# Performance work log

Measured on AMD Instinct MI355X. Metric: run time of the kernel, lower is better.

The kernel has to match this reference:

```python
import jax, jax.numpy as jnp
import numpy as np

N = 100000      # nodes
E = 1600000     # edges (avg degree 16)
IN = 128        # in_channels
H = 128         # hidden_channels
OUT = 64        # out_channels
NHID = 3        # num_layers (hidden->hidden SAGE convs)


def _lin(k, fan_out, fan_in):
    s = 1.0 / np.sqrt(fan_in)
    return jax.random.uniform(k, (fan_out, fan_in), jnp.float32, -s, s)


def setup_inputs() -> dict:
    key = jax.random.key(0)
    ks = jax.random.split(key, 12)
    x = jax.random.normal(ks[0], (N, IN), dtype=jnp.float32)
    edge_index = jax.random.randint(ks[1], (2, E), 0, N, dtype=jnp.int32)
    # inProj Linear(IN -> H)
    Wp = _lin(ks[2], H, IN)
    bp = jnp.zeros((H,), jnp.float32)
    # 3 hidden SAGEConv(H -> H): lin_l (with bias) on aggregated neighbors, lin_r (no bias) on root
    Wl_h = jnp.stack([_lin(jax.random.fold_in(ks[3], i), H, H) for i in range(NHID)])
    bl_h = jnp.zeros((NHID, H), jnp.float32)
    Wr_h = jnp.stack([_lin(jax.random.fold_in(ks[4], i), H, H) for i in range(NHID)])
    # output SAGEConv(H -> OUT)
    Wl_o = _lin(ks[5], OUT, H)
    bl_o = jnp.zeros((OUT,), jnp.float32)
    Wr_o = _lin(ks[6], OUT, H)
    return {"x": x, "edge_index": edge_index, "Wp": Wp, "bp": bp,
            "Wl_h": Wl_h, "bl_h": bl_h, "Wr_h": Wr_h,
            "Wl_o": Wl_o, "bl_o": bl_o, "Wr_o": Wr_o}


def reference(x, edge_index, Wp, bp, Wl_h, bl_h, Wr_h, Wl_o, bl_o, Wr_o):
    src, dst = edge_index[0], edge_index[1]
    ones = jnp.ones((E,), x.dtype)
    deg = jax.ops.segment_sum(ones, dst, num_segments=N)           # [N]
    inv_deg = (1.0 / jnp.maximum(deg, 1.0))[:, None]               # [N,1]

    def sage(h, Wl, bl, Wr):
        # mean aggregation of source features onto destinations (irregular gather+scatter)
        s = jax.ops.segment_sum(h[src], dst, num_segments=N)       # [N,d]
        mean = s * inv_deg
        return mean @ Wl.T + bl + h @ Wr.T

    h = x @ Wp.T + bp
    inp = h
    h = jax.nn.relu(h)
    for i in range(NHID):
        h = sage(h, Wl_h[i], bl_h[i], Wr_h[i])
        h = jax.nn.relu(h)                                          # dropout is identity in eval
        h = h + 0.2 * inp
    h = sage(h, Wl_o, bl_o, Wr_o)
    return jax.nn.log_softmax(h, axis=-1)
```

## Files before the change

### kernel.cpp

```cpp
#include <hip/hip_runtime.h>
#include <math.h>

#define N_NODES 100000
#define N_EDGES 1600000
#define NBUK 391
#define PCHUNK 8192
#define NPBLK 196
#define GBLK32 3125

typedef unsigned short u16;
typedef unsigned char u8;
typedef __bf16 bf16x8 __attribute__((ext_vector_type(8)));
typedef float f32x4 __attribute__((ext_vector_type(4)));
typedef float f32x2 __attribute__((ext_vector_type(2)));

#define OFF_RP      0u
#define OFF_INVDEG  400016u
#define OFF_BHIST   800016u
#define OFF_BBASE   801600u
#define OFF_GCUR    803200u
#define OFF_PCTR    804800u
#define OFF_PAIRS   805056u
#define OFF_COL     13605056u
#define OFF_PACK    20005056u
#define OFF_INP     20267200u
#define OFF_H       45867200u
#define OFF_H8A     71467200u
#define OFF_H8B     84267200u
#define OFF_GL      97067200u
#define OFF_GR      109867200u
#define OFF_MEAN    122667200u
#define WS_NEEDED   148267200u

#define PK_WP   0
#define PK_WL   16384
#define PK_WR   65536
#define PK_WLO  114688
#define PK_WRO  122880

__device__ __forceinline__ float bfl(unsigned u) {
  union { unsigned i; float f; } v; v.i = u << 16; return v.f;
}
__device__ __forceinline__ float bfh(unsigned u) {
  union { unsigned i; float f; } v; v.i = u & 0xFFFF0000u; return v.f;
}
__device__ __forceinline__ u16 f2b(float f) {
  union { float f; unsigned i; } v; v.f = f;
  unsigned r = (v.i + 0x7FFFu + ((v.i >> 16) & 1u)) >> 16;
  return (u16)r;
}

__global__ __launch_bounds__(256) void pack_weights_k(
    const float* __restrict__ Wp, const float* __restrict__ Wl,
    const float* __restrict__ Wr, const float* __restrict__ Wlo,
    const float* __restrict__ Wro, u16* __restrict__ P) {
  int t = blockIdx.x * 256 + threadIdx.x;
  if (t >= 16384) return;
  const float* W; u16* dst; int j; int NT;
  if (t < 2048)        { W = Wp;                    dst = P + PK_WP;                j = t;                 NT = 8; }
  else if (t < 8192)   { int m = (t - 2048) >> 11;  j = (t - 2048) & 2047;
                         W = Wl + (m << 14);        dst = P + PK_WL + (m << 14);    NT = 8; }
  else if (t < 14336)  { int m = (t - 8192) >> 11;  j = (t - 8192) & 2047;
                         W = Wr + (m << 14);        dst = P + PK_WR + (m << 14);    NT = 8; }
  else if (t < 15360)  { j = t - 14336;             W = Wlo;  dst = P + PK_WLO;     NT = 4; }
  else                 { j = t - 15360;             W = Wro;  dst = P + PK_WRO;     NT = 4; }
  int lane = j & 63;
  int nt, kt;
  if (NT == 8) { nt = (j >> 6) & 7; kt = j >> 9; }
  else         { nt = (j >> 6) & 3; kt = j >> 8; }
  int n  = nt * 16 + (lane & 15);
  int k0 = kt * 32 + ((lane >> 4) << 3);
  const float* s = W + n * 128 + k0;
  ushort4 lo = make_ushort4(f2b(s[0]), f2b(s[1]), f2b(s[2]), f2b(s[3]));
  ushort4 hi = make_ushort4(f2b(s[4]), f2b(s[5]), f2b(s[6]), f2b(s[7]));
  *(ushort4*)(dst + j * 8)     = lo;
  *(ushort4*)(dst + j * 8 + 4) = hi;
}

__global__ __launch_bounds__(256) void bhist_k(const int* __restrict__ dst,
                                               int* __restrict__ bhist) {
  __shared__ int lc[NBUK];
  int t = threadIdx.x;
  for (int i = t; i < NBUK; i += 256) lc[i] = 0;
  __syncthreads();
  int base = blockIdx.x * 4096;
#pragma unroll
  for (int r = 0; r < 16; r++) {
    int i = base + r * 256 + t;
    if (i < N_EDGES) atomicAdd(&lc[dst[i] >> 8], 1);
  }
  __syncthreads();
  for (int i = t; i < NBUK; i += 256)
    if (lc[i]) atomicAdd(&bhist[i], lc[i]);
}

__global__ __launch_bounds__(512) void bscan_k(const int* __restrict__ bhist,
                                               int* __restrict__ bbase,
                                               int* __restrict__ gcur,
                                               int* __restrict__ rp) {
  __shared__ int s[512];
  int t = threadIdx.x;
  int v = (t < NBUK) ? bhist[t] : 0;
  s[t] = v;
  __syncthreads();
  for (int off = 1; off < 512; off <<= 1) {
    int u = (t >= off) ? s[t - off] : 0;
    __syncthreads();
    s[t] += u;
    __syncthreads();
  }
  if (t < NBUK) { int e = s[t] - v; bbase[t] = e; gcur[t] = e; }
  if (t == NBUK - 1) { bbase[NBUK] = s[t]; rp[N_NODES] = s[t]; }
}

__global__ __launch_bounds__(256) void part_k(const int* __restrict__ src,
                                              const int* __restrict__ dst,
                                              int* __restrict__ gcur,
                                              uint2* __restrict__ pairs) {
  __shared__ int lcnt[NBUK + 1];
  __shared__ int lofs[512];
  __shared__ int cur[NBUK];
  __shared__ int gslot[NBUK];
  __shared__ uint2 stag[PCHUNK];
  int t = threadIdx.x;
  for (int i = t; i < NBUK + 1; i += 256) lcnt[i] = 0;
  __syncthreads();
  int base = blockIdx.x * PCHUNK;
#pragma unroll
  for (int r = 0; r < PCHUNK / 256; r++) {
    int i = base + r * 256 + t;
    if (i < N_EDGES) atomicAdd(&lcnt[dst[i] >> 8], 1);
  }
  __syncthreads();
  {
    int e1 = t + 256;
    lofs[t]  = (t  <= NBUK) ? lcnt[t]  : 0;
    lofs[e1] = (e1 <= NBUK) ? lcnt[e1] : 0;
    __syncthreads();
    for (int off = 1; off < 512; off <<= 1) {
      int a0 = (t  >= off) ? lofs[t  - off] : 0;
      int a1 = (e1 >= off) ? lofs[e1 - off] : 0;
      __syncthreads();
      lofs[t] += a0; lofs[e1] += a1;
      __syncthreads();
    }
    int o0 = lofs[t]  - ((t  <= NBUK) ? lcnt[t]  : 0);
    int o1 = lofs[e1] - ((e1 <= NBUK) ? lcnt[e1] : 0);
    __syncthreads();
    lofs[t] = o0; lofs[e1] = o1;
    __syncthreads();
  }
  for (int i = t; i < NBUK; i += 256) cur[i] = lofs[i];
  __syncthreads();
#pragma unroll
  for (int r = 0; r < PCHUNK / 256; r++) {
    int i = base + r * 256 + t;
    if (i < N_EDGES) {
      int d = dst[i];
      int slot = atomicAdd(&cur[d >> 8], 1);
      stag[slot] = make_uint2((unsigned)src[i], (unsigned)d);
    }
  }
  __syncthreads();
  for (int i = t; i < NBUK; i += 256)
    if (lcnt[i]) gslot[i] = atomicAdd(&gcur[i], lcnt[i]);
  __syncthreads();
  int total = lofs[NBUK];
  for (int p = t; p < total; p += 256) {
    uint2 pr = stag[p];
    int b = (int)(pr.y >> 8);
    pairs[gslot[b] + (p - lofs[b])] = pr;
  }
}

__global__ __launch_bounds__(256) void csr_k(const uint2* __restrict__ pairs,
                                             const int* __restrict__ bbase,
                                             int* __restrict__ rp,
                                             float* __restrict__ invdeg,
                                             int* __restrict__ col) {
  __shared__ int cnt[256];
  __shared__ int scn[256];
  __shared__ int cur[256];
  int b = blockIdx.x, t = threadIdx.x;
  int lo = bbase[b], hi = bbase[b + 1];
  cnt[t] = 0;
  __syncthreads();
  for (int p = lo + t; p < hi; p += 256)
    atomicAdd(&cnt[pairs[p].y & 255], 1);
  __syncthreads();
  int c = cnt[t];
  scn[t] = c;
  __syncthreads();
  for (int off = 1; off < 256; off <<= 1) {
    int v = (t >= off) ? scn[t - off] : 0;
    __syncthreads();
    scn[t] += v;
    __syncthreads();
  }
  int excl = scn[t] - c;
  int node = (b << 8) + t;
  if (node < N_NODES) {
    rp[node] = lo + excl;
    invdeg[node] = 1.0f / (float)(c > 1 ? c : 1);
  }
  cur[t] = lo + excl;
  __syncthreads();
  for (int p = lo + t; p < hi; p += 256) {
    uint2 pr = pairs[p];
    int slot = atomicAdd(&cur[pr.y & 255], 1);
    col[slot] = (int)pr.x;
  }
}

__global__ __launch_bounds__(256) void aggregate_row_k(
    const u8* __restrict__ h8, const int* __restrict__ rp,
    const int* __restrict__ col, const float* __restrict__ invdeg,
    u16* __restrict__ mean) {
  int tid = threadIdx.x;
  int grp = tid >> 3, lane8 = tid & 7;
  int node = blockIdx.x * 32 + grp;
  int beg = rp[node], end = rp[node + 1];
  const u8* hp = h8 + lane8 * 16;
  float a[16];
#pragma unroll
  for (int i = 0; i < 16; i++) a[i] = 0.f;
  for (int j = beg; j < end; j += 8) {
    int ci = 0;
    if (j + lane8 < end) ci = col[j + lane8];
    int cnt = end - j;
#pragma unroll
    for (int e = 0; e < 8; e++) {
      if (e < cnt) {
        int s = __shfl(ci, e, 8);
        uint4 v = *(const uint4*)(hp + (size_t)s * 128);
        f32x2 p0 = __builtin_amdgcn_cvt_pk_f32_fp8(v.x, false);
        f32x2 p1 = __builtin_amdgcn_cvt_pk_f32_fp8(v.x, true);
        f32x2 p2 = __builtin_amdgcn_cvt_pk_f32_fp8(v.y, false);
        f32x2 p3 = __builtin_amdgcn_cvt_pk_f32_fp8(v.y, true);
        f32x2 p4 = __builtin_amdgcn_cvt_pk_f32_fp8(v.z, false);
        f32x2 p5 = __builtin_amdgcn_cvt_pk_f32_fp8(v.z, true);
        f32x2 p6 = __builtin_amdgcn_cvt_pk_f32_fp8(v.w, false);
        f32x2 p7 = __builtin_amdgcn_cvt_pk_f32_fp8(v.w, true);
        a[0]  += p0[0]; a[1]  += p0[1]; a[2]  += p1[0]; a[3]  += p1[1];
        a[4]  += p2[0]; a[5]  += p2[1]; a[6]  += p3[0]; a[7]  += p3[1];
        a[8]  += p4[0]; a[9]  += p4[1]; a[10] += p5[0]; a[11] += p5[1];
        a[12] += p6[0]; a[13] += p6[1]; a[14] += p7[0]; a[15] += p7[1];
      }
    }
  }
  float wd = invdeg[node];
  u16* mp = mean + (size_t)node * 128 + lane8 * 16;
  *(ushort4*)(mp)      = make_ushort4(f2b(a[0]*wd),  f2b(a[1]*wd),  f2b(a[2]*wd),  f2b(a[3]*wd));
  *(ushort4*)(mp + 4)  = make_ushort4(f2b(a[4]*wd),  f2b(a[5]*wd),  f2b(a[6]*wd),  f2b(a[7]*wd));
  *(ushort4*)(mp + 8)  = make_ushort4(f2b(a[8]*wd),  f2b(a[9]*wd),  f2b(a[10]*wd), f2b(a[11]*wd));
  *(ushort4*)(mp + 12) = make_ushort4(f2b(a[12]*wd), f2b(a[13]*wd), f2b(a[14]*wd), f2b(a[15]*wd));
}

__global__ __launch_bounds__(256) void out_gather_k(
    const u16* __restrict__ gl, const int* __restrict__ rp,
    const int* __restrict__ col, const float* __restrict__ invdeg,
    float* __restrict__ partial) {
  int tid = threadIdx.x;
  int grp = tid >> 3, lane8 = tid & 7;
  int node = blockIdx.x * 32 + grp;
  int beg = rp[node], end = rp[node + 1];
  const u16* gp = gl + lane8 * 8;
  float a[8];
#pragma unroll
  for (int i = 0; i < 8; i++) a[i] = 0.f;
  for (int j = beg; j < end; j += 8) {
    int ci = 0;
    if (j + lane8 < end) ci = col[j + lane8];
    int cnt = end - j;
#pragma unroll
    for (int e = 0; e < 8; e++) {
      if (e < cnt) {
        int s = __shfl(ci, e, 8);
        uint4 v = *(const uint4*)(gp + (size_t)s * 64);
        a[0] += bfl(v.x); a[1] += bfh(v.x);
        a[2] += bfl(v.y); a[3] += bfh(v.y);
        a[4] += bfl(v.z); a[5] += bfh(v.z);
        a[6] += bfl(v.w); a[7] += bfh(v.w);
      }
    }
  }
  float wd = invdeg[node];
  float* pp = partial + (size_t)node * 64 + lane8 * 8;
  *(float4*)(pp)     = make_float4(a[0]*wd, a[1]*wd, a[2]*wd, a[3]*wd);
  *(float4*)(pp + 4) = make_float4(a[4]*wd, a[5]*wd, a[6]*wd, a[7]*wd);
}

__global__ __launch_bounds__(256) void out_softmax_k(
    const float* __restrict__ partial, const u16* __restrict__ gr,
    const float* __restrict__ blo, float* __restrict__ outp) {
  int node = blockIdx.x * 8 + (threadIdx.x >> 5);
  int lane = threadIdx.x & 31;
  if (node >= N_NODES) return;
  float2 pz = *(const float2*)(partial + (size_t)node * 64 + lane * 2);
  unsigned g = *(const unsigned*)(gr + (size_t)node * 64 + lane * 2);
  float z0 = pz.x + bfl(g) + blo[lane * 2];
  float z1 = pz.y + bfh(g) + blo[lane * 2 + 1];
  float mx = fmaxf(z0, z1);
#pragma unroll
  for (int off = 16; off >= 1; off >>= 1) mx = fmaxf(mx, __shfl_xor(mx, off, 32));
  float s = __expf(z0 - mx) + __expf(z1 - mx);
#pragma unroll
  for (int off = 16; off >= 1; off >>= 1) s += __shfl_xor(s, off, 32);
  float ro = mx + __logf(s);
  float2 o = make_float2(z0 - ro, z1 - ro);
  *(float2*)(outp + (size_t)node * 64 + lane * 2) = o;
}

__global__ __launch_bounds__(256) void inproj_mfma_k(
    const float* __restrict__ X, const u16* __restrict__ P,
    const float* __restrict__ bias,
    u16* __restrict__ inp, u16* __restrict__ hout, u8* __restrict__ h8out, int M) {
  __shared__ float zb[64 * 132];
  int tid = threadIdx.x;
  int w = tid >> 6, lane = tid & 63;
  int quad = lane >> 4, l15 = lane & 15;
  int m0 = blockIdx.x * 64;
  int rowa = m0 + w * 16 + l15; if (rowa > M - 1) rowa = M - 1;
  f32x4 acc[8] = {};
#pragma unroll
  for (int kt = 0; kt < 4; kt++) {
    const float* xr = X + (long)rowa * 128 + kt * 32 + quad * 8;
    float4 p0 = *(const float4*)xr;
    float4 p1 = *(const float4*)(xr + 4);
    union { ushort4 u4[2]; bf16x8 v; } fa;
    fa.u4[0] = make_ushort4(f2b(p0.x), f2b(p0.y), f2b(p0.z), f2b(p0.w));
    fa.u4[1] = make_ushort4(f2b(p1.x), f2b(p1.y), f2b(p1.z), f2b(p1.w));
    const u16* pb = P + ((kt * 8) * 64 + lane) * 8;
#pragma unroll
    for (int nt = 0; nt < 8; nt++) {
      bf16x8 bf = *(const bf16x8*)(pb + nt * 512);
      acc[nt] = __builtin_amdgcn_mfma_f32_16x16x32_bf16(fa.v, bf, acc[nt], 0, 0, 0);
    }
  }
#pragma unroll
  for (int nt = 0; nt < 8; nt++) {
    int c = nt * 16 + l15;
    float b = bias[c];
#pragma unroll
    for (int r = 0; r < 4; r++)
      zb[(w * 16 + quad * 4 + r) * 132 + c] = acc[nt][r] + b;
  }
  __syncthreads();
  int r = lane >> 2, seg = lane & 3;
  long grow = m0 + w * 16 + r;
  if (grow < M) {
    const float* zrow = &zb[(w * 16 + r) * 132 + seg * 32];
    u16* ip = inp + grow * 128 + seg * 32;
    u16* hp = hout + grow * 128 + seg * 32;
    u8*  qp = h8out + grow * 128 + seg * 32;
#pragma unroll
    for (int b = 0; b < 4; b++) {
      float zv[8];
      *(float4*)&zv[0] = *(const float4*)(zrow + b * 8);
      *(float4*)&zv[4] = *(const float4*)(zrow + b * 8 + 4);
      float rv[8];
#pragma unroll
      for (int jj = 0; jj < 8; jj++) rv[jj] = fmaxf(zv[jj], 0.f);
      *(ushort4*)(ip + b * 8)     = make_ushort4(f2b(zv[0]), f2b(zv[1]), f2b(zv[2]), f2b(zv[3]));
      *(ushort4*)(ip + b * 8 + 4) = make_ushort4(f2b(zv[4]), f2b(zv[5]), f2b(zv[6]), f2b(zv[7]));
      *(ushort4*)(hp + b * 8)     = make_ushort4(f2b(rv[0]), f2b(rv[1]), f2b(rv[2]), f2b(rv[3]));
      *(ushort4*)(hp + b * 8 + 4) = make_ushort4(f2b(rv[4]), f2b(rv[5]), f2b(rv[6]), f2b(rv[7]));
      unsigned q0 = 0, q1 = 0;
      q0 = __builtin_amdgcn_cvt_pk_fp8_f32(rv[0], rv[1], q0, false);
      q0 = __builtin_amdgcn_cvt_pk_fp8_f32(rv[2], rv[3], q0, true);
      q1 = __builtin_amdgcn_cvt_pk_fp8_f32(rv[4], rv[5], q1, false);
      q1 = __builtin_amdgcn_cvt_pk_fp8_f32(rv[6], rv[7], q1, true);
      *(uint2*)(qp + b * 8) = make_uint2(q0, q1);
    }
  }
}

__global__ __launch_bounds__(256) void sage_mfma8_k(
    const u16* __restrict__ A0, const u16* __restrict__ P0,
    const u16* __restrict__ A1, const u16* __restrict__ P1,
    const float* __restrict__ bias, const u16* __restrict__ inp,
    u16* __restrict__ outp, u8* __restrict__ h8out, int M) {
  __shared__ float zb[64 * 132];
  int tid = threadIdx.x;
  int w = tid >> 6, lane = tid & 63;
  int quad = lane >> 4, l15 = lane & 15;
  int m0 = blockIdx.x * 64;
  int rowa = m0 + w * 16 + l15; if (rowa > M - 1) rowa = M - 1;
  f32x4 acc[8] = {};
#pragma unroll
  for (int kt = 0; kt < 4; kt++) {
    bf16x8 am = *(const bf16x8*)(A0 + (long)rowa * 128 + kt * 32 + quad * 8);
    bf16x8 ar = *(const bf16x8*)(A1 + (long)rowa * 128 + kt * 32 + quad * 8);
    const u16* pl = P0 + ((kt * 8) * 64 + lane) * 8;
    const u16* pr = P1 + ((kt * 8) * 64 + lane) * 8;
#pragma unroll
    for (int nt = 0; nt < 8; nt++) {
      bf16x8 b0 = *(const bf16x8*)(pl + nt * 512);
      bf16x8 b1 = *(const bf16x8*)(pr + nt * 512);
      acc[nt] = __builtin_amdgcn_mfma_f32_16x16x32_bf16(am, b0, acc[nt], 0, 0, 0);
      acc[nt] = __builtin_amdgcn_mfma_f32_16x16x32_bf16(ar, b1, acc[nt], 0, 0, 0);
    }
  }
#pragma unroll
  for (int nt = 0; nt < 8; nt++) {
    int c = nt * 16 + l15;
    float b = bias[c];
#pragma unroll
    for (int r = 0; r < 4; r++)
      zb[(w * 16 + quad * 4 + r) * 132 + c] = fmaxf(acc[nt][r] + b, 0.f);
  }
  __syncthreads();
  int r = lane >> 2, seg = lane & 3;
  long grow = m0 + w * 16 + r;
  if (grow < M) {
    const float* zrow = &zb[(w * 16 + r) * 132 + seg * 32];
    const u16* ip = inp + grow * 128 + seg * 32;
    u16* op = outp + grow * 128 + seg * 32;
#pragma unroll
    for (int b = 0; b < 4; b++) {
      float zv[8];
      *(float4*)&zv[0] = *(const float4*)(zrow + b * 8);
      *(float4*)&zv[4] = *(const float4*)(zrow + b * 8 + 4);
      uint2 iv0 = *(const uint2*)(ip + b * 8);
      uint2 iv1 = *(const uint2*)(ip + b * 8 + 4);
      float fv[8];
      fv[0] = zv[0] + 0.2f * bfl(iv0.x); fv[1] = zv[1] + 0.2f * bfh(iv0.x);
      fv[2] = zv[2] + 0.2f * bfl(iv0.y); fv[3] = zv[3] + 0.2f * bfh(iv0.y);
      fv[4] = zv[4] + 0.2f * bfl(iv1.x); fv[5] = zv[5] + 0.2f * bfh(iv1.x);
      fv[6] = zv[6] + 0.2f * bfl(iv1.y); fv[7] = zv[7] + 0.2f * bfh(iv1.y);
      *(ushort4*)(op + b * 8)     = make_ushort4(f2b(fv[0]), f2b(fv[1]), f2b(fv[2]), f2b(fv[3]));
      *(ushort4*)(op + b * 8 + 4) = make_ushort4(f2b(fv[4]), f2b(fv[5]), f2b(fv[6]), f2b(fv[7]));
      if (h8out) {
        unsigned q0 = 0, q1 = 0;
        q0 = __builtin_amdgcn_cvt_pk_fp8_f32(fv[0], fv[1], q0, false);
        q0 = __builtin_amdgcn_cvt_pk_fp8_f32(fv[2], fv[3], q0, true);
        q1 = __builtin_amdgcn_cvt_pk_fp8_f32(fv[4], fv[5], q1, false);
        q1 = __builtin_amdgcn_cvt_pk_fp8_f32(fv[6], fv[7], q1, true);
        *(uint2*)(h8out + grow * 128 + seg * 32 + b * 8) = make_uint2(q0, q1);
      }
    }
  }
}

__global__ __launch_bounds__(256) void out_proj_k(
    const u16* __restrict__ A, const u16* __restrict__ PLO,
    const u16* __restrict__ PRO, u16* __restrict__ gl, u16* __restrict__ gr, int M) {
  __shared__ float zb[64 * 132];
  int tid = threadIdx.x;
  int w = tid >> 6, lane = tid & 63;
  int quad = lane >> 4, l15 = lane & 15;
  int m0 = blockIdx.x * 64;
  int rowa = m0 + w * 16 + l15; if (rowa > M - 1) rowa = M - 1;
  f32x4 acc[8] = {};
#pragma unroll
  for (int kt = 0; kt < 4; kt++) {
    bf16x8 af = *(const bf16x8*)(A + (long)rowa * 128 + kt * 32 + quad * 8);
#pragma unroll
    for (int nt = 0; nt < 4; nt++) {
      bf16x8 b0 = *(const bf16x8*)(PLO + ((kt * 4 + nt) * 64 + lane) * 8);
      bf16x8 b1 = *(const bf16x8*)(PRO + ((kt * 4 + nt) * 64 + lane) * 8);
      acc[nt]     = __builtin_amdgcn_mfma_f32_16x16x32_bf16(af, b0, acc[nt], 0, 0, 0);
      acc[4 + nt] = __builtin_amdgcn_mfma_f32_16x16x32_bf16(af, b1, acc[4 + nt], 0, 0, 0);
    }
  }
#pragma unroll
  for (int nt = 0; nt < 4; nt++) {
    int c = nt * 16 + l15;
#pragma unroll
    for (int r = 0; r < 4; r++) {
      zb[(w * 16 + quad * 4 + r) * 132 + c]      = acc[nt][r];
      zb[(w * 16 + quad * 4 + r) * 132 + 64 + c] = acc[4 + nt][r];
    }
  }
  __syncthreads();
  int r = lane >> 2, seg = lane & 3;
  long grow = m0 + w * 16 + r;
  if (grow < M) {
    const float* zrow = &zb[(w * 16 + r) * 132 + seg * 32];
    u16* dp = (seg < 2) ? (gl + grow * 64 + seg * 32) : (gr + grow * 64 + (seg - 2) * 32);
#pragma unroll
    for (int b = 0; b < 4; b++) {
      float zv[8];
      *(float4*)&zv[0] = *(const float4*)(zrow + b * 8);
      *(float4*)&zv[4] = *(const float4*)(zrow + b * 8 + 4);
      *(ushort4*)(dp + b * 8)     = make_ushort4(f2b(zv[0]), f2b(zv[1]), f2b(zv[2]), f2b(zv[3]));
      *(ushort4*)(dp + b * 8 + 4) = make_ushort4(f2b(zv[4]), f2b(zv[5]), f2b(zv[6]), f2b(zv[7]));
    }
  }
}

extern "C" void kernel_launch(void* const* d_in, const int* in_sizes, int n_in,
                              void* d_out, int out_size, void* d_ws, size_t ws_size,
                              hipStream_t stream) {
  if (ws_size < (size_t)WS_NEEDED) return;
  const float* x   = (const float*)d_in[0];
  const int*   ei  = (const int*)d_in[1];
  const float* Wp  = (const float*)d_in[2];
  const float* bp  = (const float*)d_in[3];
  const float* Wl  = (const float*)d_in[4];
  const float* bl  = (const float*)d_in[5];
  const float* Wr  = (const float*)d_in[6];
  const float* Wlo = (const float*)d_in[7];
  const float* blo = (const float*)d_in[8];
  const float* Wro = (const float*)d_in[9];
  float* out = (float*)d_out;
  char* ws = (char*)d_ws;
  int*   rp     = (int*)(ws + OFF_RP);
  float* invdeg = (float*)(ws + OFF_INVDEG);
  int*   bhist  = (int*)(ws + OFF_BHIST);
  int*   bbase  = (int*)(ws + OFF_BBASE);
  int*   gcur   = (int*)(ws + OFF_GCUR);
  uint2* pairs  = (uint2*)(ws + OFF_PAIRS);
  int*   col    = (int*)(ws + OFF_COL);
  u16*   pack   = (u16*)(ws + OFF_PACK);
  u16*   inp    = (u16*)(ws + OFF_INP);
  u16*   h      = (u16*)(ws + OFF_H);
  u8*    h8a    = (u8*)(ws + OFF_H8A);
  u8*    h8b    = (u8*)(ws + OFF_H8B);
  u16*   gl     = (u16*)(ws + OFF_GL);
  u16*   gr     = (u16*)(ws + OFF_GR);
  u16*   mean   = (u16*)(ws + OFF_MEAN);
  float* partial = (float*)(ws + OFF_MEAN);
  const int* srcv = ei;
  const int* dstv = ei + N_EDGES;

  hipMemsetAsync(ws + OFF_BHIST, 0, OFF_PAIRS - OFF_BHIST, stream);
  pack_weights_k<<<64, 256, 0, stream>>>(Wp, Wl, Wr, Wlo, Wro, pack);
  bhist_k<<<391, 256, 0, stream>>>(dstv, bhist);
  bscan_k<<<1, 512, 0, stream>>>(bhist, bbase, gcur, rp);
  part_k<<<NPBLK, 256, 0, stream>>>(srcv, dstv, gcur, pairs);
  csr_k<<<NBUK, 256, 0, stream>>>(pairs, bbase, rp, invdeg, col);

  int gblk = (N_NODES + 63) / 64;
  int fblk = (N_NODES + 7) / 8;

  inproj_mfma_k<<<gblk, 256, 0, stream>>>(x, pack + PK_WP, bp, inp, h, h8a, N_NODES);

  aggregate_row_k<<<GBLK32, 256, 0, stream>>>(h8a, rp, col, invdeg, mean);
  sage_mfma8_k<<<gblk, 256, 0, stream>>>(mean, pack + PK_WL, h, pack + PK_WR,
                                         bl, inp, h, h8b, N_NODES);
  aggregate_row_k<<<GBLK32, 256, 0, stream>>>(h8b, rp, col, invdeg, mean);
  sage_mfma8_k<<<gblk, 256, 0, stream>>>(mean, pack + PK_WL + 16384, h, pack + PK_WR + 16384,
                                         bl + 128, inp, h, h8a, N_NODES);
  aggregate_row_k<<<GBLK32, 256, 0, stream>>>(h8a, rp, col, invdeg, mean);
  sage_mfma8_k<<<gblk, 256, 0, stream>>>(mean, pack + PK_WL + 32768, h, pack + PK_WR + 32768,
                                         bl + 256, inp, h, (u8*)nullptr, N_NODES);

  out_proj_k<<<gblk, 256, 0, stream>>>(h, pack + PK_WLO, pack + PK_WRO, gl, gr, N_NODES);
  out_gather_k<<<GBLK32, 256, 0, stream>>>(gl, rp, col, invdeg, partial);
  out_softmax_k<<<fblk, 256, 0, stream>>>(partial, gr, blo, out);
}
```

Before: 556.4 us.

## Fuse neighbor aggregation into SAGE GEMM and plane-split output gather

Each hidden-layer SAGE step now runs as one kernel. The fp8 neighbor mean for a 64-node tile is computed into shared memory and fed straight to the MFMA GEMM, so the bf16 mean buffer no longer makes a global round trip and one launch per layer disappears. The output-layer projection writes its gl half into four 16-column planes, and a new gather kernel processes one plane per block with 2 threads per node. That gather batches 8 neighbor loads per step, aiming for better cache locality on the irregular reads. The cost is that the fused kernel has fewer blocks (64 nodes each), the gather phase has lower parallelism per block, and an extra barrier is needed before the shared buffer is reused.

```diff
diff --git a/kernel.cpp b/kernel.cpp
--- a/kernel.cpp
+++ b/kernel.cpp
@@ -6,7 +6,7 @@
 #define NBUK 391
 #define PCHUNK 8192
 #define NPBLK 196
-#define GBLK32 3125
+#define PBLK16 3128
 
 typedef unsigned short u16;
 typedef unsigned char u8;
@@ -212,184 +212,69 @@
   }
 }
 
-__global__ __launch_bounds__(256) void aggregate_row_k(
+__global__ __launch_bounds__(256) void sage_fused_k(
     const u8* __restrict__ h8, const int* __restrict__ rp,
     const int* __restrict__ col, const float* __restrict__ invdeg,
-    u16* __restrict__ mean) {
+    const u16* __restrict__ P0, const u16* __restrict__ A1,
+    const u16* __restrict__ P1, const float* __restrict__ bias,
+    const u16* __restrict__ inp, u16* __restrict__ outp,
+    u8* __restrict__ h8out, int M) {
+  __shared__ float zb[64 * 132];
+  u16* meanl = (u16*)zb;
   int tid = threadIdx.x;
-  int grp = tid >> 3, lane8 = tid & 7;
-  int node = blockIdx.x * 32 + grp;
-  int beg = rp[node], end = rp[node + 1];
-  const u8* hp = h8 + lane8 * 16;
-  float a[16];
-#pragma unroll
-  for (int i = 0; i < 16; i++) a[i] = 0.f;
-  for (int j = beg; j < end; j += 8) {
-    int ci = 0;
-    if (j + lane8 < end) ci = col[j + lane8];
-    int cnt = end - j;
-#pragma unroll
-    for (int e = 0; e < 8; e++) {
-      if (e < cnt) {
-        int s = __shfl(ci, e, 8);
-        uint4 v = *(const uint4*)(hp + (size_t)s * 128);
-        f32x2 p0 = __builtin_amdgcn_cvt_pk_f32_fp8(v.x, false);
-        f32x2 p1 = __builtin_amdgcn_cvt_pk_f32_fp8(v.x, true);
-        f32x2 p2 = __builtin_amdgcn_cvt_pk_f32_fp8(v.y, false);
-        f32x2 p3 = __builtin_amdgcn_cvt_pk_f32_fp8(v.y, true);
-        f32x2 p4 = __builtin_amdgcn_cvt_pk_f32_fp8(v.z, false);
-        f32x2 p5 = __builtin_amdgcn_cvt_pk_f32_fp8(v.z, true);
-        f32x2 p6 = __builtin_amdgcn_cvt_pk_f32_fp8(v.w, false);
-        f32x2 p7 = __builtin_amdgcn_cvt_pk_f32_fp8(v.w, true);
-        a[0]  += p0[0]; a[1]  += p0[1]; a[2]  += p1[0]; a[3]  += p1[1];
-        a[4]  += p2[0]; a[5]  += p2[1]; a[6]  += p3[0]; a[7]  += p3[1];
-        a[8]  += p4[0]; a[9]  += p4[1]; a[10] += p5[0]; a[11] += p5[1];
-        a[12] += p6[0]; a[13] += p6[1]; a[14] += p7[0]; a[15] += p7[1];
+  int m0 = blockIdx.x * 64;
+  {
+    int grp = tid >> 3, lane8 = tid & 7;
+    const u8* hp = h8 + lane8 * 16;
+#pragma unroll
+    for (int half = 0; half < 2; half++) {
+      int lrow = half * 32 + grp;
+      int node = m0 + lrow; if (node > M - 1) node = M - 1;
+      int beg = rp[node], end = rp[node + 1];
+      float a[16];
+#pragma unroll
+      for (int i = 0; i < 16; i++) a[i] = 0.f;
+      for (int j = beg; j < end; j += 8) {
+        int ci = 0;
+        if (j + lane8 < end) ci = col[j + lane8];
+        int cnt = end - j;
+#pragma unroll
+        for (int e = 0; e < 8; e++) {
+          if (e < cnt) {
+            int s = __shfl(ci, e, 8);
+            uint4 v = *(const uint4*)(hp + (size_t)(unsigned)s * 128);
+            f32x2 p0 = __builtin_amdgcn_cvt_pk_f32_fp8(v.x, false);
+            f32x2 p1 = __builtin_amdgcn_cvt_pk_f32_fp8(v.x, true);
+            f32x2 p2 = __builtin_amdgcn_cvt_pk_f32_fp8(v.y, false);
+            f32x2 p3 = __builtin_amdgcn_cvt_pk_f32_fp8(v.y, true);
+            f32x2 p4 = __builtin_amdgcn_cvt_pk_f32_fp8(v.z, false);
+            f32x2 p5 = __builtin_amdgcn_cvt_pk_f32_fp8(v.z, true);
+            f32x2 p6 = __builtin_amdgcn_cvt_pk_f32_fp8(v.w, false);
+            f32x2 p7 = __builtin_amdgcn_cvt_pk_f32_fp8(v.w, true);
+            a[0]  += p0[0]; a[1]  += p0[1]; a[2]  += p1[0]; a[3]  += p1[1];
+            a[4]  += p2[0]; a[5]  += p2[1]; a[6]  += p3[0]; a[7]  += p3[1];
+            a[8]  += p4[0]; a[9]  += p4[1]; a[10] += p5[0]; a[11] += p5[1];
+            a[12] += p6[0]; a[13] += p6[1]; a[14] += p7[0]; a[15] += p7[1];
+          }
+        }
       }
-    }
-  }
-  float wd = invdeg[node];
-  u16* mp = mean + (size_t)node * 128 + lane8 * 16;
-  *(ushort4*)(mp)      = make_ushort4(f2b(a[0]*wd),  f2b(a[1]*wd),  f2b(a[2]*wd),  f2b(a[3]*wd));
-  *(ushort4*)(mp + 4)  = make_ushort4(f2b(a[4]*wd),  f2b(a[5]*wd),  f2b(a[6]*wd),  f2b(a[7]*wd));
-  *(ushort4*)(mp + 8)  = make_ushort4(f2b(a[8]*wd),  f2b(a[9]*wd),  f2b(a[10]*wd), f2b(a[11]*wd));
-  *(ushort4*)(mp + 12) = make_ushort4(f2b(a[12]*wd), f2b(a[13]*wd), f2b(a[14]*wd), f2b(a[15]*wd));
-}
-
-__global__ __launch_bounds__(256) void out_gather_k(
-    const u16* __restrict__ gl, const int* __restrict__ rp,
-    const int* __restrict__ col, const float* __restrict__ invdeg,
-    float* __restrict__ partial) {
-  int tid = threadIdx.x;
-  int grp = tid >> 3, lane8 = tid & 7;
-  int node = blockIdx.x * 32 + grp;
-  int beg = rp[node], end = rp[node + 1];
-  const u16* gp = gl + lane8 * 8;
-  float a[8];
-#pragma unroll
-  for (int i = 0; i < 8; i++) a[i] = 0.f;
-  for (int j = beg; j < end; j += 8) {
-    int ci = 0;
-    if (j + lane8 < end) ci = col[j + lane8];
-    int cnt = end - j;
-#pragma unroll
-    for (int e = 0; e < 8; e++) {
-      if (e < cnt) {
-        int s = __shfl(ci, e, 8);
-        uint4 v = *(const uint4*)(gp + (size_t)s * 64);
-        a[0] += bfl(v.x); a[1] += bfh(v.x);
-        a[2] += bfl(v.y); a[3] += bfh(v.y);
-        a[4] += bfl(v.z); a[5] += bfh(v.z);
-        a[6] += bfl(v.w); a[7] += bfh(v.w);
-      }
-    }
-  }
-  float wd = invdeg[node];
-  float* pp = partial + (size_t)node * 64 + lane8 * 8;
-  *(float4*)(pp)     = make_float4(a[0]*wd, a[1]*wd, a[2]*wd, a[3]*wd);
-  *(float4*)(pp + 4) = make_float4(a[4]*wd, a[5]*wd, a[6]*wd, a[7]*wd);
-}
-
-__global__ __launch_bounds__(256) void out_softmax_k(
-    const float* __restrict__ partial, const u16* __restrict__ gr,
-    const float* __restrict__ blo, float* __restrict__ outp) {
-  int node = blockIdx.x * 8 + (threadIdx.x >> 5);
-  int lane = threadIdx.x & 31;
-  if (node >= N_NODES) return;
-  float2 pz = *(const float2*)(partial + (size_t)node * 64 + lane * 2);
-  unsigned g = *(const unsigned*)(gr + (size_t)node * 64 + lane * 2);
-  float z0 = pz.x + bfl(g) + blo[lane * 2];
-  float z1 = pz.y + bfh(g) + blo[lane * 2 + 1];
-  float mx = fmaxf(z0, z1);
-#pragma unroll
-  for (int off = 16; off >= 1; off >>= 1) mx = fmaxf(mx, __shfl_xor(mx, off, 32));
-  float s = __expf(z0 - mx) + __expf(z1 - mx);
-#pragma unroll
-  for (int off = 16; off >= 1; off >>= 1) s += __shfl_xor(s, off, 32);
-  float ro = mx + __logf(s);
-  float2 o = make_float2(z0 - ro, z1 - ro);
-  *(float2*)(outp + (size_t)node * 64 + lane * 2) = o;
-}
-
-__global__ __launch_bounds__(256) void inproj_mfma_k(
-    const float* __restrict__ X, const u16* __restrict__ P,
-    const float* __restrict__ bias,
-    u16* __restrict__ inp, u16* __restrict__ hout, u8* __restrict__ h8out, int M) {
-  __shared__ float zb[64 * 132];
-  int tid = threadIdx.x;
+      float wd = invdeg[node];
+      u16* mp = meanl + lrow * 136 + lane8 * 16;
+      *(ushort4*)(mp)      = make_ushort4(f2b(a[0]*wd),  f2b(a[1]*wd),  f2b(a[2]*wd),  f2b(a[3]*wd));
+      *(ushort4*)(mp + 4)  = make_ushort4(f2b(a[4]*wd),  f2b(a[5]*wd),  f2b(a[6]*wd),  f2b(a[7]*wd));
+      *(ushort4*)(mp + 8)  = make_ushort4(f2b(a[8]*wd),  f2b(a[9]*wd),  f2b(a[10]*wd), f2b(a[11]*wd));
+      *(ushort4*)(mp + 12) = make_ushort4(f2b(a[12]*wd), f2b(a[13]*wd), f2b(a[14]*wd), f2b(a[15]*wd));
+    }
+  }
+  __syncthreads();
   int w = tid >> 6, lane = tid & 63;
   int quad = lane >> 4, l15 = lane & 15;
-  int m0 = blockIdx.x * 64;
   int rowa = m0 + w * 16 + l15; if (rowa > M - 1) rowa = M - 1;
+  int lrowa = w * 16 + l15;
   f32x4 acc[8] = {};
 #pragma unroll
   for (int kt = 0; kt < 4; kt++) {
-    const float* xr = X + (long)rowa * 128 + kt * 32 + quad * 8;
-    float4 p0 = *(const float4*)xr;
-    float4 p1 = *(const float4*)(xr + 4);
-    union { ushort4 u4[2]; bf16x8 v; } fa;
-    fa.u4[0] = make_ushort4(f2b(p0.x), f2b(p0.y), f2b(p0.z), f2b(p0.w));
-    fa.u4[1] = make_ushort4(f2b(p1.x), f2b(p1.y), f2b(p1.z), f2b(p1.w));
-    const u16* pb = P + ((kt * 8) * 64 + lane) * 8;
-#pragma unroll
-    for (int nt = 0; nt < 8; nt++) {
-      bf16x8 bf = *(const bf16x8*)(pb + nt * 512);
-      acc[nt] = __builtin_amdgcn_mfma_f32_16x16x32_bf16(fa.v, bf, acc[nt], 0, 0, 0);
-    }
-  }
-#pragma unroll
-  for (int nt = 0; nt < 8; nt++) {
-    int c = nt * 16 + l15;
-    float b = bias[c];
-#pragma unroll
-    for (int r = 0; r < 4; r++)
-      zb[(w * 16 + quad * 4 + r) * 132 + c] = acc[nt][r] + b;
-  }
-  __syncthreads();
-  int r = lane >> 2, seg = lane & 3;
-  long grow = m0 + w * 16 + r;
-  if (grow < M) {
-    const float* zrow = &zb[(w * 16 + r) * 132 + seg * 32];
-    u16* ip = inp + grow * 128 + seg * 32;
-    u16* hp = hout + grow * 128 + seg * 32;
-    u8*  qp = h8out + grow * 128 + seg * 32;
-#pragma unroll
-    for (int b = 0; b < 4; b++) {
-      float zv[8];
-      *(float4*)&zv[0] = *(const float4*)(zrow + b * 8);
-      *(float4*)&zv[4] = *(const float4*)(zrow + b * 8 + 4);
-      float rv[8];
-#pragma unroll
-      for (int jj = 0; jj < 8; jj++) rv[jj] = fmaxf(zv[jj], 0.f);
-      *(ushort4*)(ip + b * 8)     = make_ushort4(f2b(zv[0]), f2b(zv[1]), f2b(zv[2]), f2b(zv[3]));
-      *(ushort4*)(ip + b * 8 + 4) = make_ushort4(f2b(zv[4]), f2b(zv[5]), f2b(zv[6]), f2b(zv[7]));
-      *(ushort4*)(hp + b * 8)     = make_ushort4(f2b(rv[0]), f2b(rv[1]), f2b(rv[2]), f2b(rv[3]));
-      *(ushort4*)(hp + b * 8 + 4) = make_ushort4(f2b(rv[4]), f2b(rv[5]), f2b(rv[6]), f2b(rv[7]));
-      unsigned q0 = 0, q1 = 0;
-      q0 = __builtin_amdgcn_cvt_pk_fp8_f32(rv[0], rv[1], q0, false);
-      q0 = __builtin_amdgcn_cvt_pk_fp8_f32(rv[2], rv[3], q0, true);
-      q1 = __builtin_amdgcn_cvt_pk_fp8_f32(rv[4], rv[5], q1, false);
-      q1 = __builtin_amdgcn_cvt_pk_fp8_f32(rv[6], rv[7], q1, true);
-      *(uint2*)(qp + b * 8) = make_uint2(q0, q1);
-    }
-  }
-}
-
-__global__ __launch_bounds__(256) void sage_mfma8_k(
-    const u16* __restrict__ A0, const u16* __restrict__ P0,
-    const u16* __restrict__ A1, const u16* __restrict__ P1,
-    const float* __restrict__ bias, const u16* __restrict__ inp,
-    u16* __restrict__ outp, u8* __restrict__ h8out, int M) {
-  __shared__ float zb[64 * 132];
-  int tid = threadIdx.x;
-  int w = tid >> 6, lane = tid & 63;
-  int quad = lane >> 4, l15 = lane & 15;
-  int m0 = blockIdx.x * 64;
-  int rowa = m0 + w * 16 + l15; if (rowa > M - 1) rowa = M - 1;
-  f32x4 acc[8] = {};
-#pragma unroll
-  for (int kt = 0; kt < 4; kt++) {
-    bf16x8 am = *(const bf16x8*)(A0 + (long)rowa * 128 + kt * 32 + quad * 8);
+    bf16x8 am = *(const bf16x8*)(meanl + lrowa * 136 + kt * 32 + quad * 8);
     bf16x8 ar = *(const bf16x8*)(A1 + (long)rowa * 128 + kt * 32 + quad * 8);
     const u16* pl = P0 + ((kt * 8) * 64 + lane) * 8;
     const u16* pr = P1 + ((kt * 8) * 64 + lane) * 8;
@@ -401,6 +286,7 @@
       acc[nt] = __builtin_amdgcn_mfma_f32_16x16x32_bf16(ar, b1, acc[nt], 0, 0, 0);
     }
   }
+  __syncthreads();
 #pragma unroll
   for (int nt = 0; nt < 8; nt++) {
     int c = nt * 16 + l15;
@@ -442,6 +328,139 @@
   }
 }
 
+__global__ __launch_bounds__(256) void out_gather16_k(
+    const u16* __restrict__ gl, const int* __restrict__ rp,
+    const int* __restrict__ col, const float* __restrict__ invdeg,
+    float* __restrict__ partial) {
+  int b = blockIdx.x;
+  int plane = (b & 7) >> 1;
+  int idx = ((b >> 3) << 1) + (b & 1);
+  int tid = threadIdx.x;
+  int grp = tid >> 1, lane2 = tid & 1;
+  int node = idx * 128 + grp;
+  if (node >= N_NODES) return;
+  int beg = rp[node], end = rp[node + 1];
+  const u16* gp = gl + (size_t)plane * (N_NODES * 16) + lane2 * 8;
+  float a[8];
+#pragma unroll
+  for (int i = 0; i < 8; i++) a[i] = 0.f;
+  int j = beg;
+  for (; j + 8 <= end; j += 8) {
+    int4 ci = *(const int4*)(col + j + lane2 * 4);
+    int cia[4] = {ci.x, ci.y, ci.z, ci.w};
+    uint4 v[8];
+#pragma unroll
+    for (int e = 0; e < 8; e++) {
+      int s = __shfl(cia[e & 3], e >> 2, 2);
+      v[e] = *(const uint4*)(gp + ((size_t)(unsigned)s << 4));
+    }
+#pragma unroll
+    for (int e = 0; e < 8; e++) {
+      a[0] += bfl(v[e].x); a[1] += bfh(v[e].x);
+      a[2] += bfl(v[e].y); a[3] += bfh(v[e].y);
+      a[4] += bfl(v[e].z); a[5] += bfh(v[e].z);
+      a[6] += bfl(v[e].w); a[7] += bfh(v[e].w);
+    }
+  }
+  for (; j < end; j++) {
+    int s = col[j];
+    uint4 vv = *(const uint4*)(gp + ((size_t)(unsigned)s << 4));
+    a[0] += bfl(vv.x); a[1] += bfh(vv.x);
+    a[2] += bfl(vv.y); a[3] += bfh(vv.y);
+    a[4] += bfl(vv.z); a[5] += bfh(vv.z);
+    a[6] += bfl(vv.w); a[7] += bfh(vv.w);
+  }
+  float wd = invdeg[node];
+  float* pp = partial + (size_t)node * 64 + plane * 16 + lane2 * 8;
+  *(float4*)(pp)     = make_float4(a[0]*wd, a[1]*wd, a[2]*wd, a[3]*wd);
+  *(float4*)(pp + 4) = make_float4(a[4]*wd, a[5]*wd, a[6]*wd, a[7]*wd);
+}
+
+__global__ __launch_bounds__(256) void out_softmax_k(
+    const float* __restrict__ partial, const u16* __restrict__ gr,
+    const float* __restrict__ blo, float* __restrict__ outp) {
+  int node = blockIdx.x * 8 + (threadIdx.x >> 5);
+  int lane = threadIdx.x & 31;
+  if (node >= N_NODES) return;
+  float2 pz = *(const float2*)(partial + (size_t)node * 64 + lane * 2);
+  unsigned g = *(const unsigned*)(gr + (size_t)node * 64 + lane * 2);
+  float z0 = pz.x + bfl(g) + blo[lane * 2];
+  float z1 = pz.y + bfh(g) + blo[lane * 2 + 1];
+  float mx = fmaxf(z0, z1);
+#pragma unroll
+  for (int off = 16; off >= 1; off >>= 1) mx = fmaxf(mx, __shfl_xor(mx, off, 32));
+  float s = __expf(z0 - mx) + __expf(z1 - mx);
+#pragma unroll
+  for (int off = 16; off >= 1; off >>= 1) s += __shfl_xor(s, off, 32);
+  float ro = mx + __logf(s);
+  float2 o = make_float2(z0 - ro, z1 - ro);
+  *(float2*)(outp + (size_t)node * 64 + lane * 2) = o;
+}
+
+__global__ __launch_bounds__(256) void inproj_mfma_k(
+    const float* __restrict__ X, const u16* __restrict__ P,
+    const float* __restrict__ bias,
+    u16* __restrict__ inp, u16* __restrict__ hout, u8* __restrict__ h8out, int M) {
+  __shared__ float zb[64 * 132];
+  int tid = threadIdx.x;
+  int w = tid >> 6, lane = tid & 63;
+  int quad = lane >> 4, l15 = lane & 15;
+  int m0 = blockIdx.x * 64;
+  int rowa = m0 + w * 16 + l15; if (rowa > M - 1) rowa = M - 1;
+  f32x4 acc[8] = {};
+#pragma unroll
+  for (int kt = 0; kt < 4; kt++) {
+    const float* xr = X + (long)rowa * 128 + kt * 32 + quad * 8;
+    float4 p0 = *(const float4*)xr;
+    float4 p1 = *(const float4*)(xr + 4);
+    union { ushort4 u4[2]; bf16x8 v; } fa;
+    fa.u4[0] = make_ushort4(f2b(p0.x), f2b(p0.y), f2b(p0.z), f2b(p0.w));
+    fa.u4[1] = make_ushort4(f2b(p1.x), f2b(p1.y), f2b(p1.z), f2b(p1.w));
+    const u16* pb = P + ((kt * 8) * 64 + lane) * 8;
+#pragma unroll
+    for (int nt = 0; nt < 8; nt++) {
+      bf16x8 bf = *(const bf16x8*)(pb + nt * 512);
+      acc[nt] = __builtin_amdgcn_mfma_f32_16x16x32_bf16(fa.v, bf, acc[nt], 0, 0, 0);
+    }
+  }
+#pragma unroll
+  for (int nt = 0; nt < 8; nt++) {
+    int c = nt * 16 + l15;
+    float b = bias[c];
+#pragma unroll
+    for (int r = 0; r < 4; r++)
+      zb[(w * 16 + quad * 4 + r) * 132 + c] = acc[nt][r] + b;
+  }
+  __syncthreads();
+  int r = lane >> 2, seg = lane & 3;
+  long grow = m0 + w * 16 + r;
+  if (grow < M) {
+    const float* zrow = &zb[(w * 16 + r) * 132 + seg * 32];
+    u16* ip = inp + grow * 128 + seg * 32;
+    u16* hp = hout + grow * 128 + seg * 32;
+    u8*  qp = h8out + grow * 128 + seg * 32;
+#pragma unroll
+    for (int b = 0; b < 4; b++) {
+      float zv[8];
+      *(float4*)&zv[0] = *(const float4*)(zrow + b * 8);
+      *(float4*)&zv[4] = *(const float4*)(zrow + b * 8 + 4);
+      float rv[8];
+#pragma unroll
+      for (int jj = 0; jj < 8; jj++) rv[jj] = fmaxf(zv[jj], 0.f);
+      *(ushort4*)(ip + b * 8)     = make_ushort4(f2b(zv[0]), f2b(zv[1]), f2b(zv[2]), f2b(zv[3]));
+      *(ushort4*)(ip + b * 8 + 4) = make_ushort4(f2b(zv[4]), f2b(zv[5]), f2b(zv[6]), f2b(zv[7]));
+      *(ushort4*)(hp + b * 8)     = make_ushort4(f2b(rv[0]), f2b(rv[1]), f2b(rv[2]), f2b(rv[3]));
+      *(ushort4*)(hp + b * 8 + 4) = make_ushort4(f2b(rv[4]), f2b(rv[5]), f2b(rv[6]), f2b(rv[7]));
+      unsigned q0 = 0, q1 = 0;
+      q0 = __builtin_amdgcn_cvt_pk_fp8_f32(rv[0], rv[1], q0, false);
+      q0 = __builtin_amdgcn_cvt_pk_fp8_f32(rv[2], rv[3], q0, true);
+      q1 = __builtin_amdgcn_cvt_pk_fp8_f32(rv[4], rv[5], q1, false);
+      q1 = __builtin_amdgcn_cvt_pk_fp8_f32(rv[6], rv[7], q1, true);
+      *(uint2*)(qp + b * 8) = make_uint2(q0, q1);
+    }
+  }
+}
+
 __global__ __launch_bounds__(256) void out_proj_k(
     const u16* __restrict__ A, const u16* __restrict__ PLO,
     const u16* __restrict__ PRO, u16* __restrict__ gl, u16* __restrict__ gr, int M) {
@@ -477,14 +496,20 @@
   long grow = m0 + w * 16 + r;
   if (grow < M) {
     const float* zrow = &zb[(w * 16 + r) * 132 + seg * 32];
-    u16* dp = (seg < 2) ? (gl + grow * 64 + seg * 32) : (gr + grow * 64 + (seg - 2) * 32);
 #pragma unroll
     for (int b = 0; b < 4; b++) {
       float zv[8];
       *(float4*)&zv[0] = *(const float4*)(zrow + b * 8);
       *(float4*)&zv[4] = *(const float4*)(zrow + b * 8 + 4);
-      *(ushort4*)(dp + b * 8)     = make_ushort4(f2b(zv[0]), f2b(zv[1]), f2b(zv[2]), f2b(zv[3]));
-      *(ushort4*)(dp + b * 8 + 4) = make_ushort4(f2b(zv[4]), f2b(zv[5]), f2b(zv[6]), f2b(zv[7]));
+      u16* dp;
+      if (seg < 2) {
+        int plane = seg * 2 + (b >> 1);
+        dp = gl + (size_t)plane * (N_NODES * 16) + grow * 16 + (b & 1) * 8;
+      } else {
+        dp = gr + grow * 64 + (seg - 2) * 32 + b * 8;
+      }
+      *(ushort4*)(dp)     = make_ushort4(f2b(zv[0]), f2b(zv[1]), f2b(zv[2]), f2b(zv[3]));
+      *(ushort4*)(dp + 4) = make_ushort4(f2b(zv[4]), f2b(zv[5]), f2b(zv[6]), f2b(zv[7]));
     }
   }
 }
@@ -519,7 +544,6 @@
   u8*    h8b    = (u8*)(ws + OFF_H8B);
   u16*   gl     = (u16*)(ws + OFF_GL);
   u16*   gr     = (u16*)(ws + OFF_GR);
-  u16*   mean   = (u16*)(ws + OFF_MEAN);
   float* partial = (float*)(ws + OFF_MEAN);
   const int* srcv = ei;
   const int* dstv = ei + N_EDGES;
@@ -536,17 +560,17 @@
 
   inproj_mfma_k<<<gblk, 256, 0, stream>>>(x, pack + PK_WP, bp, inp, h, h8a, N_NODES);
 
-  aggregate_row_k<<<GBLK32, 256, 0, stream>>>(h8a, rp, col, invdeg, mean);
-  sage_mfma8_k<<<gblk, 256, 0, stream>>>(mean, pack + PK_WL, h, pack + PK_WR,
+  sage_fused_k<<<gblk, 256, 0, stream>>>(h8a, rp, col, invdeg,
+                                         pack + PK_WL, h, pack + PK_WR,
                                          bl, inp, h, h8b, N_NODES);
-  aggregate_row_k<<<GBLK32, 256, 0, stream>>>(h8b, rp, col, invdeg, mean);
-  sage_mfma8_k<<<gblk, 256, 0, stream>>>(mean, pack + PK_WL + 16384, h, pack + PK_WR + 16384,
+  sage_fused_k<<<gblk, 256, 0, stream>>>(h8b, rp, col, invdeg,
+                                         pack + PK_WL + 16384, h, pack + PK_WR + 16384,
                                          bl + 128, inp, h, h8a, N_NODES);
-  aggregate_row_k<<<GBLK32, 256, 0, stream>>>(h8a, rp, col, invdeg, mean);
-  sage_mfma8_k<<<gblk, 256, 0, stream>>>(mean, pack + PK_WL + 32768, h, pack + PK_WR + 32768,
+  sage_fused_k<<<gblk, 256, 0, stream>>>(h8a, rp, col, invdeg,
+                                         pack + PK_WL + 32768, h, pack + PK_WR + 32768,
                                          bl + 256, inp, h, (u8*)nullptr, N_NODES);
 
   out_proj_k<<<gblk, 256, 0, stream>>>(h, pack + PK_WLO, pack + PK_WRO, gl, gr, N_NODES);
-  out_gather_k<<<GBLK32, 256, 0, stream>>>(gl, rp, col, invdeg, partial);
+  out_gather16_k<<<PBLK16, 256, 0, stream>>>(gl, rp, col, invdeg, partial);
   out_softmax_k<<<fblk, 256, 0, stream>>>(partial, gr, blo, out);
 }
```

Measured after the change: 542.6 us. -2.5%, faster.
